# Kernel optimization log

Measured on AMD Instinct MI355X. Metric: run time of the kernel, lower is better.

Reference implementation:

```python
import jax, jax.numpy as jnp
import numpy as np

D = 196; NCH = 64; H = 8; DH = 64; INNER = H * DH; MLP = 784; SEQ = 65


def _ln(x, g, b, eps=1e-5):
    m = x.mean(-1, keepdims=True)
    v = x.var(-1, keepdims=True)
    return (x - m) / jnp.sqrt(v + eps) * g + b


def setup_inputs() -> dict:
    key = jax.random.key(0)
    ks = jax.random.split(key, 12)
    f = jax.random.normal
    return dict(
        x=f(ks[0], (1, SEQ, D), dtype=jnp.float32),
        tokens=f(ks[1], (1, D), dtype=jnp.float32),
        x_pe=f(ks[2], (1, NCH, D), dtype=jnp.float32),
        conv_k=f(ks[3], (3, 3), dtype=jnp.float32) * 0.3,   # Conv2d(1,1,3) kernel
        bn_g=jnp.ones(()), bn_b=jnp.zeros(()), bn_rm=jnp.zeros(()), bn_rv=jnp.ones(()),
        fc_w1=f(ks[4], (NCH, 12)) * 0.1,
        fc_w2=f(ks[5], (12, NCH)) * 0.1,
        ln1_g=jnp.ones((D,)), ln1_b=jnp.zeros((D,)),
        ln2_g=jnp.ones((D,)), ln2_b=jnp.zeros((D,)),
        w_qkv=f(ks[6], (D, 3 * INNER)) * 0.05,
        w_out=f(ks[7], (INNER, D)) * 0.05, b_out=jnp.zeros((D,)),
        ff_w1=f(ks[8], (D, MLP)) * 0.05, ff_b1=jnp.zeros((MLP,)),
        ff_w2=f(ks[9], (MLP, D)) * 0.05, ff_b2=jnp.zeros((D,)),
    )


def reference(x, tokens, x_pe, conv_k, bn_g, bn_b, bn_rm, bn_rv,
              fc_w1, fc_w2, ln1_g, ln1_b, ln2_g, ln2_b,
              w_qkv, w_out, b_out, ff_w1, ff_b1, ff_w2, ff_b2):
    # --- per-channel Conv2d(1,1,3,p=1)+BN+ReLU, batched over all 64 rows ---
    # Each row is (1,1,1,196): height 1 with pad 1 means the top/bottom kernel
    # rows only touch zero padding, so only the middle kernel row contributes
    # -> equivalent to a 1D conv with kernel conv_k[1].
    rows = x_pe[0]                      # [64,196]
    km = conv_k[1]                      # [3]
    xp = jnp.pad(rows, ((0, 0), (1, 1)))
    conv = km[0] * xp[:, :D] + km[1] * xp[:, 1:D + 1] + km[2] * xp[:, 2:D + 2]
    bn = (conv - bn_rm) / jnp.sqrt(bn_rv + 1e-5) * bn_g + bn_b
    a = jax.nn.relu(bn)                 # [64,196]  (== x_AfterConv / a)

    # --- sort-based suppress/excitation channel gating ---
    b1 = a.mean(-1)                     # [64] adaptive avg pool
    val = jnp.sort(b1)
    idx = jnp.argsort(b1)
    middle = jnp.where((val.max() < 0) | (val.min() > 0),
                       jnp.int32(32), jnp.argmax(val > 0).astype(jnp.int32))
    rank = jnp.argsort(idx)             # rank of each channel in ascending order
    sup = rank < middle                 # channels in idx[:middle]
    l_s = middle.astype(b1.dtype)
    l_e = (NCH - middle).astype(b1.dtype)
    b2 = jnp.where(sup,
                   b1 - 1.0 / (1.0 + jnp.power(l_s, b1)),
                   b1 + 1.0 / (1.0 + jnp.power(l_e, -b1)))

    c = jax.nn.sigmoid(jax.nn.relu(b2 @ fc_w1) @ fc_w2)   # [64]
    x_att = a * c[:, None]                                  # [64,196]
    x_att = jnp.concatenate([x_att, tokens.reshape(1, D)], axis=0)[None]  # [1,65,196]

    # --- PreNorm attention ---
    h = _ln(x, ln1_g, ln1_b)
    qkv = h @ w_qkv
    q, k, v = jnp.split(qkv, 3, axis=-1)
    def heads(t):
        return t.reshape(1, SEQ, H, DH).transpose(0, 2, 1, 3)  # b h n d
    q, k, v = heads(q), heads(k), heads(v)
    attn = jax.nn.softmax(jnp.einsum('bhnd,bhmd->bhnm', q, k) * (DH ** -0.5), axis=-1)
    o = jnp.einsum('bhnm,bhmd->bhnd', attn, v).transpose(0, 2, 1, 3).reshape(1, SEQ, INNER)
    x = o @ w_out + b_out + x + x_att

    # --- PreNorm feed-forward ---
    h2 = _ln(x, ln2_g, ln2_b)
    x = (jax.nn.gelu(h2 @ ff_w1 + ff_b1, approximate=False) @ ff_w2 + ff_b2) + x
    return x
```

## Files before the change

### kernel.cpp

```cpp
#include <hip/hip_runtime.h>
#include <math.h>

#define D 196
#define NCH 64
#define NH 8
#define DHD 64
#define INNER 512
#define MLP 784
#define SEQ 65

__device__ __forceinline__ float bsum(float v, float* red) {
    for (int off = 32; off > 0; off >>= 1) v += __shfl_down(v, off, 64);
    int lane = threadIdx.x & 63, wid = threadIdx.x >> 6;
    if (lane == 0) red[wid] = v;
    __syncthreads();
    float s = red[0] + red[1] + red[2] + red[3];
    __syncthreads();
    return s;
}

__global__ void __launch_bounds__(256) k1(const float* __restrict__ x_pe,
        const float* __restrict__ conv_k, const float* __restrict__ bn_g,
        const float* __restrict__ bn_b, const float* __restrict__ bn_rm,
        const float* __restrict__ bn_rv, const float* __restrict__ x,
        const float* __restrict__ ln1_g, const float* __restrict__ ln1_b,
        const float* __restrict__ w_qkv,
        float* __restrict__ a, float* __restrict__ b1, float* __restrict__ qkv,
        float* __restrict__ out, float* __restrict__ x2g) {
    __shared__ float red[4];
    __shared__ float h[D];
    __shared__ float ps[512];
    int b = blockIdx.x, t = threadIdx.x;
    if (b < NCH) {
        int zi = b * 200 + t;
        if (t < 200 && zi < SEQ * D) { out[zi] = 0.f; x2g[zi] = 0.f; }
        const float* row = x_pe + b * D;
        float val = 0.f;
        if (t < D) {
            float km0 = conv_k[3], km1 = conv_k[4], km2 = conv_k[5];
            float inv = rsqrtf(bn_rv[0] + 1e-5f);
            float l = (t > 0) ? row[t - 1] : 0.f;
            float m = row[t];
            float r = (t < D - 1) ? row[t + 1] : 0.f;
            float conv = km0 * l + km1 * m + km2 * r;
            float bn = (conv - bn_rm[0]) * inv * bn_g[0] + bn_b[0];
            val = fmaxf(bn, 0.f);
            a[b * D + t] = val;
        }
        float tot = bsum(val, red);
        if (t == 0) b1[b] = tot * (1.f / (float)D);
    } else {
        int qb = b - NCH;
        int n = qb / 12, cg = qb % 12;
        const float* row = x + n * D;
        float v = (t < D) ? row[t] : 0.f;
        float mean = bsum(v, red) * (1.f / (float)D);
        float d = (t < D) ? (v - mean) : 0.f;
        float var = bsum(d * d, red) * (1.f / (float)D);
        float rinv = rsqrtf(var + 1e-5f);
        if (t < D) h[t] = d * rinv * ln1_g[t] + ln1_b[t];
        __syncthreads();
        int qq = t >> 6, lt = t & 63;
        int c0 = cg * 128 + lt * 2;
        const float* wp = w_qkv + (qq * 49) * 1536 + c0;
        const float* hp = h + qq * 49;
        float a0 = 0.f, a1 = 0.f;
#pragma unroll
        for (int i = 0; i < 49; i++) {
            float2 w2 = *(const float2*)(wp + i * 1536);
            float hv = hp[i];
            a0 += hv * w2.x;
            a1 += hv * w2.y;
        }
        ps[qq * 128 + lt * 2] = a0;
        ps[qq * 128 + lt * 2 + 1] = a1;
        __syncthreads();
        if (t < 64) {
            float s0 = ps[t * 2] + ps[128 + t * 2] + ps[256 + t * 2] + ps[384 + t * 2];
            float s1 = ps[t * 2 + 1] + ps[129 + t * 2] + ps[257 + t * 2] + ps[385 + t * 2];
            float2 o2 = make_float2(s0, s1);
            *(float2*)(qkv + n * 1536 + cg * 128 + t * 2) = o2;
        }
    }
}

__global__ void __launch_bounds__(256) k2(const float* __restrict__ b1,
        const float* __restrict__ fc_w1, const float* __restrict__ fc_w2,
        const float* __restrict__ qkv, const float* __restrict__ w_out,
        const float* __restrict__ b_out, const float* __restrict__ x,
        const float* __restrict__ a, const float* __restrict__ tokens,
        float* __restrict__ x2g) {
    __shared__ float sq[128];
    __shared__ float pp[2 * 80];
    __shared__ float so[128];
    __shared__ float ps[784];
    __shared__ float sb1[NCH];
    __shared__ float sb2[NCH];
    __shared__ float hid[12];
    __shared__ float cgate;

    int n = blockIdx.x, g = blockIdx.y, t = threadIdx.x;
    int w = t >> 6, L = t & 63;

    if (t < 128) sq[t] = qkv[n * 1536 + g * 128 + t];

    if (g == 0) {
        if (t < NCH) {
            sb1[t] = b1[t];
            float v = b1[t];
            float mx = -1e30f, mn = 1e30f;
            int cle = 0, rank = 0;
            for (int j = 0; j < NCH; j++) {
                float ww = sb1[j];
                mx = fmaxf(mx, ww);
                mn = fminf(mn, ww);
                if (ww <= 0.f) cle++;
                if (ww < v || (ww == v && j < t)) rank++;
            }
            int middle;
            if (mx < 0.f || mn > 0.f) middle = 32;
            else if (mx <= 0.f) middle = 0;
            else middle = cle;
            float b2;
            if (rank < middle) {
                float ls = (float)middle;
                b2 = v - 1.f / (1.f + powf(ls, v));
            } else {
                float le = (float)(NCH - middle);
                b2 = v + 1.f / (1.f + powf(le, -v));
            }
            sb2[t] = b2;
        }
        if (t < 12) {
            float s = 0.f;
            for (int j = 0; j < NCH; j++) s += sb2[j] * fc_w1[j * 12 + t];
            hid[t] = fmaxf(s, 0.f);
        }
        if (t == 0 && n < NCH) {
            float s = 0.f;
            for (int k = 0; k < 12; k++) s += hid[k] * fc_w2[k * NCH + n];
            cgate = 1.f / (1.f + expf(-s));
        }
    }

    if (t < 128) {
        int head = g * 2 + w;
        const float scale = 0.125f;
        const float4* kr = (const float4*)(qkv + L * 1536 + INNER + head * DHD);
        const float4* q4 = (const float4*)(sq + w * DHD);
        float s = 0.f;
#pragma unroll
        for (int i = 0; i < 16; i++) {
            float4 kv = kr[i];
            float4 qv = q4[i];
            s += qv.x * kv.x + qv.y * kv.y + qv.z * kv.z + qv.w * kv.w;
        }
        float sL = s * scale;
        float t64 = sq[w * DHD + L] * qkv[64 * 1536 + INNER + head * DHD + L];
#pragma unroll
        for (int off = 1; off < 64; off <<= 1) t64 += __shfl_xor(t64, off, 64);
        float s64 = t64 * scale;
        float mx = sL;
#pragma unroll
        for (int off = 1; off < 64; off <<= 1) mx = fmaxf(mx, __shfl_xor(mx, off, 64));
        mx = fmaxf(mx, s64);
        float e = expf(sL - mx);
        float e64 = expf(s64 - mx);
        float esum = e;
#pragma unroll
        for (int off = 1; off < 64; off <<= 1) esum += __shfl_xor(esum, off, 64);
        esum += e64;
        float rs = 1.f / esum;
        pp[w * 80 + L] = e;
        if (L == 0) pp[w * 80 + 64] = e64;
        float acc = 0.f;
#pragma unroll 13
        for (int m = 0; m < SEQ; m++)
            acc += pp[w * 80 + m] * qkv[m * 1536 + 2 * INNER + head * DHD + L];
        so[w * DHD + L] = acc * rs;
    }
    __syncthreads();

    if (t < 196) {
        int qq = t / 49, p = t - qq * 49;
        const float* wp = w_out + (g * 128 + qq * 32) * D + 4 * p;
        const float* op = so + qq * 32;
        float a0 = 0.f, a1 = 0.f, a2 = 0.f, a3 = 0.f;
#pragma unroll
        for (int i = 0; i < 32; i++) {
            float4 w4 = *(const float4*)(wp + i * D);
            float ov = op[i];
            a0 += ov * w4.x;
            a1 += ov * w4.y;
            a2 += ov * w4.z;
            a3 += ov * w4.w;
        }
        ps[qq * 196 + 4 * p]     = a0;
        ps[qq * 196 + 4 * p + 1] = a1;
        ps[qq * 196 + 4 * p + 2] = a2;
        ps[qq * 196 + 4 * p + 3] = a3;
    }
    __syncthreads();
    if (t < 196) {
        float sacc = ps[t] + ps[196 + t] + ps[392 + t] + ps[588 + t];
        if (g == 0) {
            float att = (n < NCH) ? a[n * D + t] * cgate : tokens[t];
            sacc += x[n * D + t] + b_out[t] + att;
        }
        atomicAdd(&x2g[n * D + t], sacc);
    }
}

__global__ void __launch_bounds__(256) k3(const float* __restrict__ x2g,
        const float* __restrict__ ln2_g, const float* __restrict__ ln2_b,
        const float* __restrict__ ff_w1, const float* __restrict__ ff_b1,
        const float* __restrict__ ff_w2, const float* __restrict__ ff_b2,
        float* __restrict__ out) {
    __shared__ float red[4];
    __shared__ float x2s[D];
    __shared__ float h2s[D];
    __shared__ float st[49];
    __shared__ float ps[196];
    int n = blockIdx.x, cg = blockIdx.y, t = threadIdx.x;
    float v = 0.f;
    if (t < D) { v = x2g[n * D + t]; x2s[t] = v; }
    float mean = bsum(v, red) * (1.f / (float)D);
    float d = (t < D) ? (v - mean) : 0.f;
    float var = bsum(d * d, red) * (1.f / (float)D);
    float rinv = rsqrtf(var + 1e-5f);
    if (t < D) h2s[t] = d * rinv * ln2_g[t] + ln2_b[t];
    __syncthreads();
    if (t < 196) {
        int qq = t / 49, p = t - qq * 49;
        int c0 = cg * 49 + p;
        const float* wp = ff_w1 + (qq * 49) * MLP + c0;
        const float* hp = h2s + qq * 49;
        float a0 = 0.f;
#pragma unroll
        for (int i = 0; i < 49; i++) a0 += hp[i] * wp[i * MLP];
        ps[qq * 49 + p] = a0;
    }
    __syncthreads();
    if (t < 49) {
        float s0 = ps[t] + ps[49 + t] + ps[98 + t] + ps[147 + t] + ff_b1[cg * 49 + t];
        st[t] = 0.5f * s0 * (1.f + erff(s0 * 0.70710678118f));
    }
    __syncthreads();
    if (t < D) {
        const float* wp = ff_w2 + (cg * 49) * D + t;
        float s = 0.f;
#pragma unroll
        for (int i = 0; i < 49; i++) s += st[i] * wp[i * D];
        if (cg == 0) s += ff_b2[t] + x2s[t];
        atomicAdd(&out[n * D + t], s);
    }
}

extern "C" void kernel_launch(void* const* d_in, const int* in_sizes, int n_in,
                              void* d_out, int out_size, void* d_ws, size_t ws_size,
                              hipStream_t stream) {
    const float* x      = (const float*)d_in[0];
    const float* tokens = (const float*)d_in[1];
    const float* x_pe   = (const float*)d_in[2];
    const float* conv_k = (const float*)d_in[3];
    const float* bn_g   = (const float*)d_in[4];
    const float* bn_b   = (const float*)d_in[5];
    const float* bn_rm  = (const float*)d_in[6];
    const float* bn_rv  = (const float*)d_in[7];
    const float* fc_w1  = (const float*)d_in[8];
    const float* fc_w2  = (const float*)d_in[9];
    const float* ln1_g  = (const float*)d_in[10];
    const float* ln1_b  = (const float*)d_in[11];
    const float* ln2_g  = (const float*)d_in[12];
    const float* ln2_b  = (const float*)d_in[13];
    const float* w_qkv  = (const float*)d_in[14];
    const float* w_out  = (const float*)d_in[15];
    const float* b_out  = (const float*)d_in[16];
    const float* ff_w1  = (const float*)d_in[17];
    const float* ff_b1  = (const float*)d_in[18];
    const float* ff_w2  = (const float*)d_in[19];
    const float* ff_b2  = (const float*)d_in[20];
    float* out = (float*)d_out;

    float* ws = (float*)d_ws;
    float* a    = ws;
    float* b1   = ws + 12544;
    float* qkv  = ws + 12608;
    float* x2g  = ws + 112448;

    k1<<<844, 256, 0, stream>>>(x_pe, conv_k, bn_g, bn_b, bn_rm, bn_rv,
                                x, ln1_g, ln1_b, w_qkv, a, b1, qkv, out, x2g);
    k2<<<dim3(SEQ, 4), 256, 0, stream>>>(b1, fc_w1, fc_w2, qkv, w_out, b_out,
                                         x, a, tokens, x2g);
    k3<<<dim3(SEQ, 16), 256, 0, stream>>>(x2g, ln2_g, ln2_b,
                                          ff_w1, ff_b1, ff_w2, ff_b2, out);
}
```

Before: 126.7 us.

## Fuse three kernels into one cooperative persistent kernel with grid syncs

```diff
diff --git a/kernel.cpp b/kernel.cpp
--- a/kernel.cpp
+++ b/kernel.cpp
@@ -1,4 +1,5 @@
 #include <hip/hip_runtime.h>
+#include <hip/hip_cooperative_groups.h>
 #include <math.h>
 
 #define D 196
@@ -8,6 +9,9 @@
 #define INNER 512
 #define MLP 784
 #define SEQ 65
+#define GRID 512
+
+namespace cgn = cooperative_groups;
 
 __device__ __forceinline__ float bsum(float v, float* red) {
     for (int off = 32; off > 0; off >>= 1) v += __shfl_down(v, off, 64);
@@ -18,6 +22,7 @@
     __syncthreads();
     return s;
 }
+
 
 __global__ void __launch_bounds__(256) k1(const float* __restrict__ x_pe,
         const float* __restrict__ conv_k, const float* __restrict__ bn_g,
@@ -256,6 +261,247 @@
     }
 }
 
+__global__ void __launch_bounds__(256, 2) fused(
+        const float* __restrict__ x_pe, const float* __restrict__ conv_k,
+        const float* __restrict__ bn_g, const float* __restrict__ bn_b,
+        const float* __restrict__ bn_rm, const float* __restrict__ bn_rv,
+        const float* __restrict__ x, const float* __restrict__ ln1_g,
+        const float* __restrict__ ln1_b, const float* __restrict__ w_qkv,
+        const float* __restrict__ fc_w1, const float* __restrict__ fc_w2,
+        const float* __restrict__ w_out, const float* __restrict__ b_out,
+        const float* __restrict__ tokens, const float* __restrict__ ln2_g,
+        const float* __restrict__ ln2_b, const float* __restrict__ ff_w1,
+        const float* __restrict__ ff_b1, const float* __restrict__ ff_w2,
+        const float* __restrict__ ff_b2,
+        float* __restrict__ a, float* __restrict__ b1, float* __restrict__ qkv,
+        float* __restrict__ x2g, float* __restrict__ out) {
+    cgn::grid_group gg = cgn::this_grid();
+    __shared__ float redA[4];
+    __shared__ float hA[D];
+    __shared__ float psA[512];
+    __shared__ float sq[128];
+    __shared__ float pp[2 * 80];
+    __shared__ float so[128];
+    __shared__ float psB[784];
+    __shared__ float sb1[NCH];
+    __shared__ float sb2[NCH];
+    __shared__ float hid[12];
+    __shared__ float cgate;
+    __shared__ float x2s[D];
+    __shared__ float h2s[D];
+    __shared__ float st[49];
+    __shared__ float psC[196];
+
+    int b = blockIdx.x, t = threadIdx.x;
+
+    for (int u = b; u < 844; u += GRID) {
+        __syncthreads();
+        if (u < NCH) {
+            int zi = u * 200 + t;
+            if (t < 200 && zi < SEQ * D) { out[zi] = 0.f; x2g[zi] = 0.f; }
+            const float* row = x_pe + u * D;
+            float val = 0.f;
+            if (t < D) {
+                float km0 = conv_k[3], km1 = conv_k[4], km2 = conv_k[5];
+                float inv = rsqrtf(bn_rv[0] + 1e-5f);
+                float l = (t > 0) ? row[t - 1] : 0.f;
+                float m = row[t];
+                float r = (t < D - 1) ? row[t + 1] : 0.f;
+                float conv = km0 * l + km1 * m + km2 * r;
+                float bn = (conv - bn_rm[0]) * inv * bn_g[0] + bn_b[0];
+                val = fmaxf(bn, 0.f);
+                a[u * D + t] = val;
+            }
+            float tot = bsum(val, redA);
+            if (t == 0) b1[u] = tot * (1.f / (float)D);
+        } else {
+            int qb = u - NCH;
+            int n = qb / 12, cg = qb % 12;
+            const float* row = x + n * D;
+            float v = (t < D) ? row[t] : 0.f;
+            float mean = bsum(v, redA) * (1.f / (float)D);
+            float d = (t < D) ? (v - mean) : 0.f;
+            float var = bsum(d * d, redA) * (1.f / (float)D);
+            float rinv = rsqrtf(var + 1e-5f);
+            if (t < D) hA[t] = d * rinv * ln1_g[t] + ln1_b[t];
+            __syncthreads();
+            int qq = t >> 6, lt = t & 63;
+            int c0 = cg * 128 + lt * 2;
+            const float* wp = w_qkv + (qq * 49) * 1536 + c0;
+            const float* hp = hA + qq * 49;
+            float a0 = 0.f, a1 = 0.f;
+#pragma unroll
+            for (int i = 0; i < 49; i++) {
+                float2 w2 = *(const float2*)(wp + i * 1536);
+                float hv = hp[i];
+                a0 += hv * w2.x;
+                a1 += hv * w2.y;
+            }
+            psA[qq * 128 + lt * 2] = a0;
+            psA[qq * 128 + lt * 2 + 1] = a1;
+            __syncthreads();
+            if (t < 64) {
+                float s0 = psA[t * 2] + psA[128 + t * 2] + psA[256 + t * 2] + psA[384 + t * 2];
+                float s1 = psA[t * 2 + 1] + psA[129 + t * 2] + psA[257 + t * 2] + psA[385 + t * 2];
+                float2 o2 = make_float2(s0, s1);
+                *(float2*)(qkv + n * 1536 + cg * 128 + t * 2) = o2;
+            }
+        }
+    }
+    gg.sync();
+
+    if (b < 260) {
+        int n = b >> 2, g = b & 3;
+        int w = t >> 6, L = t & 63;
+
+        if (t < 128) sq[t] = qkv[n * 1536 + g * 128 + t];
+
+        if (g == 0) {
+            if (t < NCH) {
+                sb1[t] = b1[t];
+                float v = b1[t];
+                float mx = -1e30f, mn = 1e30f;
+                int cle = 0, rank = 0;
+                for (int j = 0; j < NCH; j++) {
+                    float ww = sb1[j];
+                    mx = fmaxf(mx, ww);
+                    mn = fminf(mn, ww);
+                    if (ww <= 0.f) cle++;
+                    if (ww < v || (ww == v && j < t)) rank++;
+                }
+                int middle;
+                if (mx < 0.f || mn > 0.f) middle = 32;
+                else if (mx <= 0.f) middle = 0;
+                else middle = cle;
+                float b2;
+                if (rank < middle) {
+                    float ls = (float)middle;
+                    b2 = v - 1.f / (1.f + powf(ls, v));
+                } else {
+                    float le = (float)(NCH - middle);
+                    b2 = v + 1.f / (1.f + powf(le, -v));
+                }
+                sb2[t] = b2;
+            }
+            if (t < 12) {
+                float s = 0.f;
+                for (int j = 0; j < NCH; j++) s += sb2[j] * fc_w1[j * 12 + t];
+                hid[t] = fmaxf(s, 0.f);
+            }
+            if (t == 0 && n < NCH) {
+                float s = 0.f;
+                for (int k = 0; k < 12; k++) s += hid[k] * fc_w2[k * NCH + n];
+                cgate = 1.f / (1.f + expf(-s));
+            }
+        }
+
+        if (t < 128) {
+            int head = g * 2 + w;
+            const float scale = 0.125f;
+            const float4* kr = (const float4*)(qkv + L * 1536 + INNER + head * DHD);
+            const float4* q4 = (const float4*)(sq + w * DHD);
+            float s = 0.f;
+#pragma unroll
+            for (int i = 0; i < 16; i++) {
+                float4 kv = kr[i];
+                float4 qv = q4[i];
+                s += qv.x * kv.x + qv.y * kv.y + qv.z * kv.z + qv.w * kv.w;
+            }
+            float sL = s * scale;
+            float t64 = sq[w * DHD + L] * qkv[64 * 1536 + INNER + head * DHD + L];
+#pragma unroll
+            for (int off = 1; off < 64; off <<= 1) t64 += __shfl_xor(t64, off, 64);
+            float s64 = t64 * scale;
+            float mx = sL;
+#pragma unroll
+            for (int off = 1; off < 64; off <<= 1) mx = fmaxf(mx, __shfl_xor(mx, off, 64));
+            mx = fmaxf(mx, s64);
+            float e = expf(sL - mx);
+            float e64 = expf(s64 - mx);
+            float esum = e;
+#pragma unroll
+            for (int off = 1; off < 64; off <<= 1) esum += __shfl_xor(esum, off, 64);
+            esum += e64;
+            float rs = 1.f / esum;
+            pp[w * 80 + L] = e;
+            if (L == 0) pp[w * 80 + 64] = e64;
+            float acc = 0.f;
+#pragma unroll 13
+            for (int m = 0; m < SEQ; m++)
+                acc += pp[w * 80 + m] * qkv[m * 1536 + 2 * INNER + head * DHD + L];
+            so[w * DHD + L] = acc * rs;
+        }
+        __syncthreads();
+
+        if (t < 196) {
+            int qq = t / 49, p = t - qq * 49;
+            const float* wp = w_out + (g * 128 + qq * 32) * D + 4 * p;
+            const float* op = so + qq * 32;
+            float a0 = 0.f, a1 = 0.f, a2 = 0.f, a3 = 0.f;
+#pragma unroll
+            for (int i = 0; i < 32; i++) {
+                float4 w4 = *(const float4*)(wp + i * D);
+                float ov = op[i];
+                a0 += ov * w4.x;
+                a1 += ov * w4.y;
+                a2 += ov * w4.z;
+                a3 += ov * w4.w;
+            }
+            psB[qq * 196 + 4 * p]     = a0;
+            psB[qq * 196 + 4 * p + 1] = a1;
+            psB[qq * 196 + 4 * p + 2] = a2;
+            psB[qq * 196 + 4 * p + 3] = a3;
+        }
+        __syncthreads();
+        if (t < 196) {
+            float sacc = psB[t] + psB[196 + t] + psB[392 + t] + psB[588 + t];
+            if (g == 0) {
+                float att = (n < NCH) ? a[n * D + t] * cgate : tokens[t];
+                sacc += x[n * D + t] + b_out[t] + att;
+            }
+            atomicAdd(&x2g[n * D + t], sacc);
+        }
+    }
+    gg.sync();
+
+    for (int u = b; u < SEQ * 16; u += GRID) {
+        __syncthreads();
+        int n = u >> 4, fg = u & 15;
+        float v = 0.f;
+        if (t < D) { v = x2g[n * D + t]; x2s[t] = v; }
+        float mean = bsum(v, redA) * (1.f / (float)D);
+        float d = (t < D) ? (v - mean) : 0.f;
+        float var = bsum(d * d, redA) * (1.f / (float)D);
+        float rinv = rsqrtf(var + 1e-5f);
+        if (t < D) h2s[t] = d * rinv * ln2_g[t] + ln2_b[t];
+        __syncthreads();
+        if (t < 196) {
+            int qq = t / 49, p = t - qq * 49;
+            int c0 = fg * 49 + p;
+            const float* wp = ff_w1 + (qq * 49) * MLP + c0;
+            const float* hp = h2s + qq * 49;
+            float a0 = 0.f;
+#pragma unroll
+            for (int i = 0; i < 49; i++) a0 += hp[i] * wp[i * MLP];
+            psC[qq * 49 + p] = a0;
+        }
+        __syncthreads();
+        if (t < 49) {
+            float s0 = psC[t] + psC[49 + t] + psC[98 + t] + psC[147 + t] + ff_b1[fg * 49 + t];
+            st[t] = 0.5f * s0 * (1.f + erff(s0 * 0.70710678118f));
+        }
+        __syncthreads();
+        if (t < D) {
+            const float* wp = ff_w2 + (fg * 49) * D + t;
+            float s = 0.f;
+#pragma unroll
+            for (int i = 0; i < 49; i++) s += st[i] * wp[i * D];
+            if (fg == 0) s += ff_b2[t] + x2s[t];
+            atomicAdd(&out[n * D + t], s);
+        }
+    }
+}
+
 extern "C" void kernel_launch(void* const* d_in, const int* in_sizes, int n_in,
                               void* d_out, int out_size, void* d_ws, size_t ws_size,
                               hipStream_t stream) {
@@ -288,10 +534,20 @@
     float* qkv  = ws + 12608;
     float* x2g  = ws + 112448;
 
-    k1<<<844, 256, 0, stream>>>(x_pe, conv_k, bn_g, bn_b, bn_rm, bn_rv,
-                                x, ln1_g, ln1_b, w_qkv, a, b1, qkv, out, x2g);
-    k2<<<dim3(SEQ, 4), 256, 0, stream>>>(b1, fc_w1, fc_w2, qkv, w_out, b_out,
-                                         x, a, tokens, x2g);
-    k3<<<dim3(SEQ, 16), 256, 0, stream>>>(x2g, ln2_g, ln2_b,
-                                          ff_w1, ff_b1, ff_w2, ff_b2, out);
+    void* kargs[] = {
+        (void*)&x_pe, (void*)&conv_k, (void*)&bn_g, (void*)&bn_b, (void*)&bn_rm,
+        (void*)&bn_rv, (void*)&x, (void*)&ln1_g, (void*)&ln1_b, (void*)&w_qkv,
+        (void*)&fc_w1, (void*)&fc_w2, (void*)&w_out, (void*)&b_out, (void*)&tokens,
+        (void*)&ln2_g, (void*)&ln2_b, (void*)&ff_w1, (void*)&ff_b1, (void*)&ff_w2,
+        (void*)&ff_b2, (void*)&a, (void*)&b1, (void*)&qkv, (void*)&x2g, (void*)&out};
+    hipError_t err = hipLaunchCooperativeKernel((const void*)fused, dim3(GRID),
+                                                dim3(256), kargs, 0, stream);
+    if (err != hipSuccess) {
+        k1<<<844, 256, 0, stream>>>(x_pe, conv_k, bn_g, bn_b, bn_rm, bn_rv,
+                                    x, ln1_g, ln1_b, w_qkv, a, b1, qkv, out, x2g);
+        k2<<<dim3(SEQ, 4), 256, 0, stream>>>(b1, fc_w1, fc_w2, qkv, w_out, b_out,
+                                             x, a, tokens, x2g);
+        k3<<<dim3(SEQ, 16), 256, 0, stream>>>(x2g, ln2_g, ln2_b,
+                                              ff_w1, ff_b1, ff_w2, ff_b2, out);
+    }
 }
```

After: 277.8 us. 2.19x slower.
